# Kernel optimization log

Hardware: AMD Instinct MI355X
Metric: run time of the kernel (lower is better)

Reference implementation:

```python
import jax, jax.numpy as jnp
import numpy as np

B_SZ, T, N, H = 8, 4096, 256, 512  # batch, seq, num_neurons, d_hidden
RMAX, RMIN = 0.99, 0.4


def _glorot_half(k, shape):
    # VarianceScaling(scale=0.5, mode='fan_avg', distribution='uniform')
    fan_avg = (shape[0] + shape[1]) / 2.0
    limit = float(np.sqrt(3.0 * 0.5 / fan_avg))
    return jax.random.uniform(k, shape, jnp.float32, -limit, limit)


def setup_inputs() -> dict:
    key = jax.random.key(0)
    ks = jax.random.split(key, 8)
    x = jax.random.normal(ks[0], (B_SZ, T, N), jnp.float32)
    C_re = _glorot_half(ks[1], (H, N))
    C_im = _glorot_half(ks[2], (H, N))
    B_re = _glorot_half(ks[3], (N, H))
    B_im = _glorot_half(ks[4], (N, H))
    D = jax.random.normal(ks[5], (N,), jnp.float32)
    numin = float(np.log(-np.log(RMAX)))
    numax = float(np.log(-np.log(RMIN)))
    nu = jax.random.uniform(ks[6], (H,), jnp.float32, numin, numax)
    theta = jax.random.uniform(ks[7], (H,), jnp.float32, 0.0, 3.14 / 10)
    lam_abs = jnp.exp(-jnp.exp(nu))  # |lambda| = |exp(-exp(nu) + i*theta)|
    gamma_log = jnp.log(jnp.sqrt(1.0 - lam_abs ** 2))
    return dict(x=x, B_re=B_re, B_im=B_im, C_re=C_re, C_im=C_im,
                D=D, nu=nu, theta=theta, gamma_log=gamma_log)


def _binary_op(qi, qj):
    A_i, b_i = qi
    A_j, b_j = qj
    return (A_j * A_i, A_j * b_i + b_j)


def reference(x, B_re, B_im, C_re, C_im, D, nu, theta, gamma_log):
    u = x  # adapter is identity since n_in == num_neurons
    lam_log = jax.lax.complex(-jnp.exp(nu), theta)            # (H,) log-lambda
    lam = jnp.exp(lam_log)                                     # (H,) diagonal transition
    gamma = jnp.exp(gamma_log).astype(jnp.complex64)           # (H,)
    Bm = jax.lax.complex(B_re, B_im)                           # (N,H)
    Cm = jax.lax.complex(C_re, C_im)                           # (H,N)
    u_c = u.astype(jnp.complex64)
    bu = gamma * (u_c @ Bm)                                    # (B,T,H) complex64
    A = jnp.broadcast_to(lam, (1, u.shape[1], lam.shape[0]))   # (1,T,H), broadcasts in op
    _, xs = jax.lax.associative_scan(_binary_op, (A, bu), axis=1)  # (B,T,H)
    y = jnp.real(xs @ Cm) + D * u                              # (B,T,N) float32
    return y
```

## Files before the change

### kernel.cpp

```cpp
#include <hip/hip_runtime.h>

#define B_SZ 8
#define T_LEN 4096
#define N_DIM 256
#define H_DIM 512
#define NC 32
#define CL 128
#define ROWS (B_SZ * T_LEN)

#define BM 128
#define BN 128
#define BKg 32

typedef __attribute__((ext_vector_type(4))) float f32x4;
typedef __attribute__((ext_vector_type(8))) short bf16x8;

static __device__ __forceinline__ unsigned short f2bf(float f) {
    unsigned int u = __float_as_uint(f);
    unsigned int r = (u + 0x7FFFu + ((u >> 16) & 1u)) >> 16;
    return (unsigned short)r;
}
static __device__ __forceinline__ float bf2f(unsigned short s) {
    return __uint_as_float(((unsigned int)s) << 16);
}

static __device__ __forceinline__ void lam_of(const float* __restrict__ nu,
                                              const float* __restrict__ theta,
                                              int h, float& lre, float& lim) {
    float r = __expf(-__expf(nu[h]));
    float th = theta[h];
    lre = r * __cosf(th);
    lim = r * __sinf(th);
}

__global__ __launch_bounds__(256) void conv_x(const float4* __restrict__ x, ushort4* __restrict__ xb) {
    int id = blockIdx.x * 256 + threadIdx.x;
    float4 v = x[id];
    ushort4 o;
    o.x = f2bf(v.x); o.y = f2bf(v.y); o.z = f2bf(v.z); o.w = f2bf(v.w);
    xb[id] = o;
}

__global__ __launch_bounds__(256) void conv_Bt(const float* __restrict__ Bre,
                                               const float* __restrict__ Bim,
                                               unsigned short* __restrict__ BT1) {
    int id = blockIdx.x * 256 + threadIdx.x;
    int k = id >> 9, h = id & 511;
    BT1[(long)(2 * h) * 256 + k]     = f2bf(Bre[id]);
    BT1[(long)(2 * h + 1) * 256 + k] = f2bf(Bim[id]);
}

__global__ __launch_bounds__(256) void conv_Ct(const float* __restrict__ Cre,
                                               const float* __restrict__ Cim,
                                               unsigned short* __restrict__ CT) {
    int id = blockIdx.x * 256 + threadIdx.x;
    int h = id >> 8, nn = id & 255;
    CT[(long)nn * 1024 + 2 * h]     = f2bf(Cre[id]);
    CT[(long)nn * 1024 + 2 * h + 1] = f2bf(-Cim[id]);
}

template <int MODE>
__global__ __launch_bounds__(256) void gemm_mfma(const unsigned short* __restrict__ A,
                                                 const unsigned short* __restrict__ Bt,
                                                 int M, int N, int K,
                                                 const float* __restrict__ e0,
                                                 const float* __restrict__ e1,
                                                 const unsigned short* __restrict__ e1b,
                                                 void* __restrict__ out) {
    __shared__ unsigned short As[BM * BKg];
    __shared__ unsigned short Bs[BN * BKg];
    const int tid = threadIdx.x;
    const int lane = tid & 63;
    const int wave = tid >> 6;
    const int wr = wave >> 1, wc = wave & 1;

    const int nwg = (int)gridDim.x;
    const int cpx = nwg >> 3;
    const int bid = (int)blockIdx.x;
    const int tile = (bid & 7) * cpx + (bid >> 3);

    const int nTilesN = N / BN;
    const long tileM = (long)(tile / nTilesN) * BM;
    const long tileN = (long)(tile % nTilesN) * BN;

    f32x4 acc[4][4] = {};

    const int fb = lane * 16;
    for (int k0 = 0; k0 < K; k0 += BKg) {
        __syncthreads();
#pragma unroll
        for (int cc = 0; cc < 2; ++cc) {
            const int c = wave + cc * 4;
            const int flat = c * 1024 + fb;
            const int row = flat >> 6;
            const int ke = (flat & 63) >> 1;
            const unsigned short* ga = A + (tileM + row) * (long)K + k0 + ke;
            __builtin_amdgcn_global_load_lds((const __attribute__((address_space(1))) unsigned int*)ga,
                                             (__attribute__((address_space(3))) unsigned int*)(As + c * 512),
                                             16, 0, 0);
            const unsigned short* gb = Bt + (tileN + row) * (long)K + k0 + ke;
            __builtin_amdgcn_global_load_lds((const __attribute__((address_space(1))) unsigned int*)gb,
                                             (__attribute__((address_space(3))) unsigned int*)(Bs + c * 512),
                                             16, 0, 0);
        }
        __syncthreads();

        bf16x8 af[4], bfr[4];
#pragma unroll
        for (int m = 0; m < 4; ++m) {
            const int row = wr * 64 + m * 16 + (lane & 15);
            af[m] = *(const bf16x8*)((const char*)As + row * 64 + 16 * (lane >> 4));
        }
#pragma unroll
        for (int n = 0; n < 4; ++n) {
            const int row = wc * 64 + n * 16 + (lane & 15);
            bfr[n] = *(const bf16x8*)((const char*)Bs + row * 64 + 16 * (lane >> 4));
        }
#pragma unroll
        for (int m = 0; m < 4; ++m)
#pragma unroll
            for (int n = 0; n < 4; ++n)
                acc[m][n] = __builtin_amdgcn_mfma_f32_16x16x32_bf16(af[m], bfr[n], acc[m][n], 0, 0, 0);
    }

    if constexpr (MODE == 0) {
        unsigned short* o = (unsigned short*)out;
#pragma unroll
        for (int n = 0; n < 4; ++n) {
            const int gcol = (int)tileN + wc * 64 + n * 16 + (lane & 15);
            const float g = __expf(e0[gcol >> 1]);
#pragma unroll
            for (int m = 0; m < 4; ++m) {
                const long grow0 = tileM + wr * 64 + m * 16 + ((lane >> 4) << 2);
#pragma unroll
                for (int r = 0; r < 4; ++r)
                    o[(grow0 + r) * N + gcol] = f2bf(acc[m][n][r] * g);
            }
        }
    } else {
        float* o = (float*)out;
#pragma unroll
        for (int n = 0; n < 4; ++n) {
            const int gcol = (int)tileN + wc * 64 + n * 16 + (lane & 15);
            const float dv = e0[gcol];
#pragma unroll
            for (int m = 0; m < 4; ++m) {
                const long grow0 = tileM + wr * 64 + m * 16 + ((lane >> 4) << 2);
#pragma unroll
                for (int r = 0; r < 4; ++r) {
                    const long idx = (grow0 + r) * N + gcol;
                    const float uv = e1b ? bf2f(e1b[idx]) : e1[idx];
                    o[idx] = acc[m][n][r] + dv * uv;
                }
            }
        }
    }
}


__global__ __launch_bounds__(256) void k2s_sums(const ushort4* __restrict__ xs4,
                                                float4* __restrict__ sums,
                                                const float* __restrict__ nu,
                                                const float* __restrict__ theta) {
    const int gid = blockIdx.x * 256 + threadIdx.x;
    const int hp = gid & 255;
    const int c = (gid >> 8) & (NC - 1);
    const int b = gid >> 13;
    float lre0, lim0, lre1, lim1;
    lam_of(nu, theta, 2 * hp, lre0, lim0);
    lam_of(nu, theta, 2 * hp + 1, lre1, lim1);
    long base = ((long)b * T_LEN + (long)c * CL) * 256 + hp;
    float a0r = 0.f, a0i = 0.f, a1r = 0.f, a1i = 0.f;
#pragma unroll 4
    for (int i = 0; i < CL; ++i) {
        ushort4 v = xs4[base + (long)i * 256];
        float u0r = bf2f(v.x), u0i = bf2f(v.y), u1r = bf2f(v.z), u1i = bf2f(v.w);
        float n0r = fmaf(lre0, a0r, fmaf(-lim0, a0i, u0r));
        float n0i = fmaf(lre0, a0i, fmaf(lim0, a0r, u0i));
        float n1r = fmaf(lre1, a1r, fmaf(-lim1, a1i, u1r));
        float n1i = fmaf(lre1, a1i, fmaf(lim1, a1r, u1i));
        a0r = n0r; a0i = n0i; a1r = n1r; a1i = n1i;
    }
    sums[((long)b * NC + c) * 256 + hp] = make_float4(a0r, a0i, a1r, a1i);
}

__global__ __launch_bounds__(256) void k2b_carry(const float4* __restrict__ sums,
                                                 float4* __restrict__ carry,
                                                 const float* __restrict__ nu,
                                                 const float* __restrict__ theta) {
    const int gid = blockIdx.x * 256 + threadIdx.x;
    const int hp = gid & 255;
    const int b = gid >> 8;
    float lre0, lim0, lre1, lim1;
    lam_of(nu, theta, 2 * hp, lre0, lim0);
    lam_of(nu, theta, 2 * hp + 1, lre1, lim1);
    float p0r = lre0, p0i = lim0, p1r = lre1, p1i = lim1;
#pragma unroll
    for (int i = 0; i < 7; ++i) {
        float t0 = p0r * p0r - p0i * p0i; p0i = 2.f * p0r * p0i; p0r = t0;
        float t1 = p1r * p1r - p1i * p1i; p1i = 2.f * p1r * p1i; p1r = t1;
    }
    float c0r = 0.f, c0i = 0.f, c1r = 0.f, c1i = 0.f;
    for (int c = 0; c < NC; ++c) {
        long idx = ((long)b * NC + c) * 256 + hp;
        carry[idx] = make_float4(c0r, c0i, c1r, c1i);
        float4 s = sums[idx];
        float t0 = fmaf(p0r, c0r, fmaf(-p0i, c0i, s.x));
        c0i = fmaf(p0r, c0i, fmaf(p0i, c0r, s.y));
        c0r = t0;
        float t1 = fmaf(p1r, c1r, fmaf(-p1i, c1i, s.z));
        c1i = fmaf(p1r, c1i, fmaf(p1i, c1r, s.w));
        c1r = t1;
    }
}

__global__ __launch_bounds__(256) void k2ac_scan(ushort4* __restrict__ xs4,
                                                 const float4* __restrict__ carry,
                                                 const float* __restrict__ nu,
                                                 const float* __restrict__ theta) {
    const int gid = blockIdx.x * 256 + threadIdx.x;
    const int hp = gid & 255;
    const int c = (gid >> 8) & (NC - 1);
    const int b = gid >> 13;
    float lre0, lim0, lre1, lim1;
    lam_of(nu, theta, 2 * hp, lre0, lim0);
    lam_of(nu, theta, 2 * hp + 1, lre1, lim1);
    float4 cr = carry[((long)b * NC + c) * 256 + hp];
    float a0r = cr.x, a0i = cr.y, a1r = cr.z, a1i = cr.w;
    long base = ((long)b * T_LEN + (long)c * CL) * 256 + hp;
#pragma unroll 4
    for (int i = 0; i < CL; ++i) {
        ushort4 v = xs4[base + (long)i * 256];
        float u0r = bf2f(v.x), u0i = bf2f(v.y), u1r = bf2f(v.z), u1i = bf2f(v.w);
        float n0r = fmaf(lre0, a0r, fmaf(-lim0, a0i, u0r));
        float n0i = fmaf(lre0, a0i, fmaf(lim0, a0r, u0i));
        float n1r = fmaf(lre1, a1r, fmaf(-lim1, a1i, u1r));
        float n1i = fmaf(lre1, a1i, fmaf(lim1, a1r, u1i));
        a0r = n0r; a0i = n0i; a1r = n1r; a1i = n1i;
        ushort4 o;
        o.x = f2bf(a0r); o.y = f2bf(a0i); o.z = f2bf(a1r); o.w = f2bf(a1i);
        xs4[base + (long)i * 256] = o;
    }
}

extern "C" void kernel_launch(void* const* d_in, const int* in_sizes, int n_in,
                              void* d_out, int out_size, void* d_ws, size_t ws_size,
                              hipStream_t stream) {
    const float* x         = (const float*)d_in[0];
    const float* Bre       = (const float*)d_in[1];
    const float* Bim       = (const float*)d_in[2];
    const float* Cre       = (const float*)d_in[3];
    const float* Cim       = (const float*)d_in[4];
    const float* Dv        = (const float*)d_in[5];
    const float* nu        = (const float*)d_in[6];
    const float* theta     = (const float*)d_in[7];
    const float* gamma_log = (const float*)d_in[8];
    float* y = (float*)d_out;

    const size_t XS_BYTES  = (size_t)ROWS * H_DIM * 4;
    const size_t REG_BYTES = 2u * 1024 * 1024;
    const size_t XB_BYTES  = (size_t)ROWS * N_DIM * 2;
    unsigned short* xs_us = (unsigned short*)d_ws;
    ushort4* xs4   = (ushort4*)d_ws;
    char* regionA  = (char*)d_ws + XS_BYTES;
    char* regionB  = regionA + REG_BYTES;
    unsigned short* BT1 = (unsigned short*)regionA;
    float4*  sums  = (float4*)regionA;
    unsigned short* CT  = (unsigned short*)regionA;
    float4*  carry = (float4*)regionB;

    const bool xb_in_ws = ws_size >= XS_BYTES + 2 * REG_BYTES + XB_BYTES;
    unsigned short* xb = xb_in_ws ? (unsigned short*)(regionB + REG_BYTES)
                                  : (unsigned short*)d_out;

    conv_x<<<ROWS * N_DIM / 4 / 256, 256, 0, stream>>>((const float4*)x, (ushort4*)xb);
    conv_Bt<<<(N_DIM * H_DIM) / 256, 256, 0, stream>>>(Bre, Bim, BT1);

    gemm_mfma<0><<<(ROWS / BM) * (1024 / BN), 256, 0, stream>>>(xb, BT1, ROWS, 1024, 256,
                                                                gamma_log, nullptr, nullptr, xs_us);
    k2s_sums<<<(B_SZ * NC * 256) / 256, 256, 0, stream>>>(xs4, sums, nu, theta);
    k2b_carry<<<(B_SZ * 256) / 256, 256, 0, stream>>>(sums, carry, nu, theta);
    k2ac_scan<<<(B_SZ * NC * 256) / 256, 256, 0, stream>>>(xs4, carry, nu, theta);

    conv_Ct<<<(H_DIM * N_DIM) / 256, 256, 0, stream>>>(Cre, Cim, CT);

    gemm_mfma<1><<<(ROWS / BM) * (256 / BN), 256, 0, stream>>>(xs_us, CT, ROWS, 256, 1024,
                                                               Dv, x, xb_in_ws ? xb : nullptr, y);
}
```

Measured before the change: 135.1 us.

## Triple-buffer GEMM LDS tiles with async prefetch and XOR-swizzled layout

Replaces the single-buffered LDS staging in the MFMA GEMM with a three-stage ring buffer. Global-to-LDS loads for tile k+2 are issued before computing tile k, with explicit vmcnt waits and raw barriers so memory latency overlaps MFMA work. The global source columns and the LDS read offsets are also XOR-swizzled to reduce LDS bank conflicts on fragment reads. This triples LDS use per block, which may lower occupancy, and the hand-tuned waitcnt counts depend on each stage issuing exactly four loads per thread.

```diff
diff --git a/kernel.cpp b/kernel.cpp
--- a/kernel.cpp
+++ b/kernel.cpp
@@ -67,8 +67,8 @@
                                                  const float* __restrict__ e1,
                                                  const unsigned short* __restrict__ e1b,
                                                  void* __restrict__ out) {
-    __shared__ unsigned short As[BM * BKg];
-    __shared__ unsigned short Bs[BN * BKg];
+    __shared__ unsigned short As[3][BM * BKg];
+    __shared__ unsigned short Bs[3][BN * BKg];
     const int tid = threadIdx.x;
     const int lane = tid & 63;
     const int wave = tid >> 6;
@@ -83,44 +83,71 @@
     const long tileM = (long)(tile / nTilesN) * BM;
     const long tileN = (long)(tile % nTilesN) * BN;
 
-    f32x4 acc[4][4] = {};
-
-    const int fb = lane * 16;
-    for (int k0 = 0; k0 < K; k0 += BKg) {
-        __syncthreads();
+    const int rsub = lane >> 2;
+    const int sg = 8 * ((lane & 3) ^ ((lane >> 3) & 3));
+    const unsigned short* Abase = A + tileM * (long)K + sg;
+    const unsigned short* Bbase = Bt + tileN * (long)K + sg;
+
+    auto stage = [&](int buf, int k0) {
 #pragma unroll
         for (int cc = 0; cc < 2; ++cc) {
             const int c = wave + cc * 4;
-            const int flat = c * 1024 + fb;
-            const int row = flat >> 6;
-            const int ke = (flat & 63) >> 1;
-            const unsigned short* ga = A + (tileM + row) * (long)K + k0 + ke;
+            const int row = c * 16 + rsub;
+            const unsigned short* ga = Abase + (long)row * K + k0;
             __builtin_amdgcn_global_load_lds((const __attribute__((address_space(1))) unsigned int*)ga,
-                                             (__attribute__((address_space(3))) unsigned int*)(As + c * 512),
+                                             (__attribute__((address_space(3))) unsigned int*)(As[buf] + c * 512),
                                              16, 0, 0);
-            const unsigned short* gb = Bt + (tileN + row) * (long)K + k0 + ke;
+            const unsigned short* gb = Bbase + (long)row * K + k0;
             __builtin_amdgcn_global_load_lds((const __attribute__((address_space(1))) unsigned int*)gb,
-                                             (__attribute__((address_space(3))) unsigned int*)(Bs + c * 512),
+                                             (__attribute__((address_space(3))) unsigned int*)(Bs[buf] + c * 512),
                                              16, 0, 0);
         }
-        __syncthreads();
+    };
+
+    const int rdA = 16 * ((lane >> 4) ^ ((lane >> 1) & 3));
+
+    f32x4 acc[4][4] = {};
+    const int nt = K / BKg;
+
+    stage(0, 0);
+    stage(1, BKg);
+
+    int cur = 0, pf = 2;
+    for (int t = 0; t < nt; ++t) {
+        if (t + 2 < nt) {
+            stage(pf, (t + 2) * BKg);
+            asm volatile("s_waitcnt vmcnt(8)" ::: "memory");
+        } else if (t + 1 < nt) {
+            asm volatile("s_waitcnt vmcnt(4)" ::: "memory");
+        } else {
+            asm volatile("s_waitcnt vmcnt(0)" ::: "memory");
+        }
+        __builtin_amdgcn_s_barrier();
+        asm volatile("" ::: "memory");
 
         bf16x8 af[4], bfr[4];
 #pragma unroll
         for (int m = 0; m < 4; ++m) {
             const int row = wr * 64 + m * 16 + (lane & 15);
-            af[m] = *(const bf16x8*)((const char*)As + row * 64 + 16 * (lane >> 4));
+            af[m] = *(const bf16x8*)((const char*)As[cur] + row * 64 + rdA);
         }
 #pragma unroll
         for (int n = 0; n < 4; ++n) {
             const int row = wc * 64 + n * 16 + (lane & 15);
-            bfr[n] = *(const bf16x8*)((const char*)Bs + row * 64 + 16 * (lane >> 4));
+            bfr[n] = *(const bf16x8*)((const char*)Bs[cur] + row * 64 + rdA);
         }
 #pragma unroll
         for (int m = 0; m < 4; ++m)
 #pragma unroll
             for (int n = 0; n < 4; ++n)
                 acc[m][n] = __builtin_amdgcn_mfma_f32_16x16x32_bf16(af[m], bfr[n], acc[m][n], 0, 0, 0);
+
+        asm volatile("" ::: "memory");
+        __builtin_amdgcn_s_barrier();
+        asm volatile("" ::: "memory");
+
+        cur = (cur == 2) ? 0 : cur + 1;
+        pf = (pf == 2) ? 0 : pf + 1;
     }
 
     if constexpr (MODE == 0) {
```

Result: faster. 130.4 us (-3.4%).

## Load MFMA operands directly from global memory instead of staging through LDS

Applied to the files above, without the earlier changes.

Both GEMMs now have each wave read its bf16 MFMA fragments straight from global memory into registers, with the K depth fixed at compile time and the loop unrolled. The LDS tiles, the global_load_lds staging and the two barriers per K step are removed. The cost is that operands shared across waves are fetched once per wave rather than once per block, so reuse relies on L1/L2, and each lane's loads are strided and less coalesced.

```diff
diff --git a/kernel.cpp b/kernel.cpp
--- a/kernel.cpp
+++ b/kernel.cpp
@@ -8,10 +8,6 @@
 #define CL 128
 #define ROWS (B_SZ * T_LEN)
 
-#define BM 128
-#define BN 128
-#define BKg 32
-
 typedef __attribute__((ext_vector_type(4))) float f32x4;
 typedef __attribute__((ext_vector_type(8))) short bf16x8;
 
@@ -59,16 +55,14 @@
     CT[(long)nn * 1024 + 2 * h + 1] = f2bf(-Cim[id]);
 }
 
-template <int MODE>
-__global__ __launch_bounds__(256) void gemm_mfma(const unsigned short* __restrict__ A,
-                                                 const unsigned short* __restrict__ Bt,
-                                                 int M, int N, int K,
-                                                 const float* __restrict__ e0,
-                                                 const float* __restrict__ e1,
-                                                 const unsigned short* __restrict__ e1b,
-                                                 void* __restrict__ out) {
-    __shared__ unsigned short As[BM * BKg];
-    __shared__ unsigned short Bs[BN * BKg];
+template <int MODE, int KC>
+__global__ __launch_bounds__(256) void gemm_direct(const unsigned short* __restrict__ A,
+                                                   const unsigned short* __restrict__ Bt,
+                                                   int N,
+                                                   const float* __restrict__ e0,
+                                                   const float* __restrict__ e1,
+                                                   const unsigned short* __restrict__ e1b,
+                                                   void* __restrict__ out) {
     const int tid = threadIdx.x;
     const int lane = tid & 63;
     const int wave = tid >> 6;
@@ -79,43 +73,29 @@
     const int bid = (int)blockIdx.x;
     const int tile = (bid & 7) * cpx + (bid >> 3);
 
-    const int nTilesN = N / BN;
-    const long tileM = (long)(tile / nTilesN) * BM;
-    const long tileN = (long)(tile % nTilesN) * BN;
+    const int nTilesN = N / 128;
+    const long tileM = (long)(tile / nTilesN) * 128;
+    const long tileN = (long)(tile % nTilesN) * 128;
+
+    const int fr = lane & 15;
+    const int fs = lane >> 4;
+    const unsigned short* ap = A + (tileM + wr * 64 + fr) * (long)KC + fs * 8;
+    const unsigned short* bp = Bt + (tileN + wc * 64 + fr) * (long)KC + fs * 8;
 
     f32x4 acc[4][4] = {};
 
-    const int fb = lane * 16;
-    for (int k0 = 0; k0 < K; k0 += BKg) {
-        __syncthreads();
-#pragma unroll
-        for (int cc = 0; cc < 2; ++cc) {
-            const int c = wave + cc * 4;
-            const int flat = c * 1024 + fb;
-            const int row = flat >> 6;
-            const int ke = (flat & 63) >> 1;
-            const unsigned short* ga = A + (tileM + row) * (long)K + k0 + ke;
-            __builtin_amdgcn_global_load_lds((const __attribute__((address_space(1))) unsigned int*)ga,
-                                             (__attribute__((address_space(3))) unsigned int*)(As + c * 512),
-                                             16, 0, 0);
-            const unsigned short* gb = Bt + (tileN + row) * (long)K + k0 + ke;
-            __builtin_amdgcn_global_load_lds((const __attribute__((address_space(1))) unsigned int*)gb,
-                                             (__attribute__((address_space(3))) unsigned int*)(Bs + c * 512),
-                                             16, 0, 0);
-        }
-        __syncthreads();
-
+    constexpr int NT = KC / 32;
+#if 1
+#pragma unroll (KC == 256 ? 8 : 8)
+#endif
+    for (int t = 0; t < NT; ++t) {
         bf16x8 af[4], bfr[4];
 #pragma unroll
-        for (int m = 0; m < 4; ++m) {
-            const int row = wr * 64 + m * 16 + (lane & 15);
-            af[m] = *(const bf16x8*)((const char*)As + row * 64 + 16 * (lane >> 4));
-        }
-#pragma unroll
-        for (int n = 0; n < 4; ++n) {
-            const int row = wc * 64 + n * 16 + (lane & 15);
-            bfr[n] = *(const bf16x8*)((const char*)Bs + row * 64 + 16 * (lane >> 4));
-        }
+        for (int m = 0; m < 4; ++m)
+            af[m] = *(const bf16x8*)(ap + (long)m * 16 * KC + t * 32);
+#pragma unroll
+        for (int n = 0; n < 4; ++n)
+            bfr[n] = *(const bf16x8*)(bp + (long)n * 16 * KC + t * 32);
 #pragma unroll
         for (int m = 0; m < 4; ++m)
 #pragma unroll
@@ -127,11 +107,11 @@
         unsigned short* o = (unsigned short*)out;
 #pragma unroll
         for (int n = 0; n < 4; ++n) {
-            const int gcol = (int)tileN + wc * 64 + n * 16 + (lane & 15);
+            const int gcol = (int)tileN + wc * 64 + n * 16 + fr;
             const float g = __expf(e0[gcol >> 1]);
 #pragma unroll
             for (int m = 0; m < 4; ++m) {
-                const long grow0 = tileM + wr * 64 + m * 16 + ((lane >> 4) << 2);
+                const long grow0 = tileM + wr * 64 + m * 16 + (fs << 2);
 #pragma unroll
                 for (int r = 0; r < 4; ++r)
                     o[(grow0 + r) * N + gcol] = f2bf(acc[m][n][r] * g);
@@ -141,11 +121,11 @@
         float* o = (float*)out;
 #pragma unroll
         for (int n = 0; n < 4; ++n) {
-            const int gcol = (int)tileN + wc * 64 + n * 16 + (lane & 15);
+            const int gcol = (int)tileN + wc * 64 + n * 16 + fr;
             const float dv = e0[gcol];
 #pragma unroll
             for (int m = 0; m < 4; ++m) {
-                const long grow0 = tileM + wr * 64 + m * 16 + ((lane >> 4) << 2);
+                const long grow0 = tileM + wr * 64 + m * 16 + (fs << 2);
 #pragma unroll
                 for (int r = 0; r < 4; ++r) {
                     const long idx = (grow0 + r) * N + gcol;
@@ -276,14 +256,14 @@
     conv_x<<<ROWS * N_DIM / 4 / 256, 256, 0, stream>>>((const float4*)x, (ushort4*)xb);
     conv_Bt<<<(N_DIM * H_DIM) / 256, 256, 0, stream>>>(Bre, Bim, BT1);
 
-    gemm_mfma<0><<<(ROWS / BM) * (1024 / BN), 256, 0, stream>>>(xb, BT1, ROWS, 1024, 256,
-                                                                gamma_log, nullptr, nullptr, xs_us);
+    gemm_direct<0, 256><<<(ROWS / 128) * (1024 / 128), 256, 0, stream>>>(
+        xb, BT1, 1024, gamma_log, nullptr, nullptr, xs_us);
     k2s_sums<<<(B_SZ * NC * 256) / 256, 256, 0, stream>>>(xs4, sums, nu, theta);
     k2b_carry<<<(B_SZ * 256) / 256, 256, 0, stream>>>(sums, carry, nu, theta);
     k2ac_scan<<<(B_SZ * NC * 256) / 256, 256, 0, stream>>>(xs4, carry, nu, theta);
 
     conv_Ct<<<(H_DIM * N_DIM) / 256, 256, 0, stream>>>(Cre, Cim, CT);
 
-    gemm_mfma<1><<<(ROWS / BM) * (256 / BN), 256, 0, stream>>>(xs_us, CT, ROWS, 256, 1024,
-                                                               Dv, x, xb_in_ws ? xb : nullptr, y);
-}
+    gemm_direct<1, 1024><<<(ROWS / 128) * (256 / 128), 256, 0, stream>>>(
+        xs_us, CT, 256, Dv, x, xb_in_ws ? xb : nullptr, y);
+}
```

New measurement: 202.3 us. 49.8% more time.
